# Kernel optimization log

Measured on AMD Instinct MI355X. Metric: run time of the kernel, lower is better.

Reference implementation:

```python
import jax, jax.numpy as jnp
import numpy as np

EPS = 1e-5


def _dwconv(x, w, pad):
    # x: [N,C,H,W]; w: [C,1,k,k] depthwise kernel (groups = C)
    return jax.lax.conv_general_dilated(
        x, w, window_strides=(1, 1), padding=[(pad, pad), (pad, pad)],
        feature_group_count=w.shape[0],
        dimension_numbers=("NCHW", "OIHW", "NCHW"))


def _bn(y, g, b, m, v):
    # inference-mode BatchNorm2d using running stats; per-channel affine
    scale = (g / jnp.sqrt(v + EPS))[None, :, None, None]
    shift = (b - m * g / jnp.sqrt(v + EPS))[None, :, None, None]
    return y * scale + shift


def setup_inputs() -> dict:
    key = jax.random.key(0)
    ks = jax.random.split(key, 16)
    C, KL, KS = 384, 13, 3
    N, H, W = 16, 64, 64
    inp = {
        "x": jax.random.normal(ks[0], (N, C, H, W), jnp.float32),
        "w_large": jax.random.normal(ks[1], (C, 1, KL, KL), jnp.float32) * 0.05,
        "w_small": jax.random.normal(ks[2], (C, 1, KS, KS), jnp.float32) * 0.2,
        "g_l": jax.random.normal(ks[3], (C,), jnp.float32),
        "b_l": jax.random.normal(ks[4], (C,), jnp.float32),
        "m_l": jax.random.normal(ks[5], (C,), jnp.float32),
        "v_l": jax.random.uniform(ks[6], (C,), jnp.float32, 0.5, 1.5),
        "g_s": jax.random.normal(ks[7], (C,), jnp.float32),
        "b_s": jax.random.normal(ks[8], (C,), jnp.float32),
        "m_s": jax.random.normal(ks[9], (C,), jnp.float32),
        "v_s": jax.random.uniform(ks[10], (C,), jnp.float32, 0.5, 1.5),
        "g_i": jax.random.normal(ks[11], (C,), jnp.float32),
        "b_i": jax.random.normal(ks[12], (C,), jnp.float32),
        "m_i": jax.random.normal(ks[13], (C,), jnp.float32),
        "v_i": jax.random.uniform(ks[14], (C,), jnp.float32, 0.5, 1.5),
    }
    return inp


def reference(x, w_large, w_small, g_l, b_l, m_l, v_l,
              g_s, b_s, m_s, v_s, g_i, b_i, m_i, v_i):
    kl = w_large.shape[-1]
    ks = w_small.shape[-1]
    out = (_bn(_dwconv(x, w_large, kl // 2), g_l, b_l, m_l, v_l)
           + _bn(_dwconv(x, w_small, ks // 2), g_s, b_s, m_s, v_s)
           + _bn(x, g_i, b_i, m_i, v_i))
    return out
```

## Files before the change

### kernel.cpp

```cpp
#include <hip/hip_runtime.h>

#define EPSV 1e-5f

typedef __fp16 f16x8 __attribute__((ext_vector_type(8)));
typedef float f32x4 __attribute__((ext_vector_type(4)));
typedef __fp16 half2v __attribute__((ext_vector_type(2)));

__device__ __forceinline__ unsigned h2_as_u32(half2v h) {
    union { half2v h; unsigned u; } cv;
    cv.h = h;
    return cv.u;
}

#define LROWS 76
#define LSTRIDE 88

__global__ __launch_bounds__(256) void fuse_weights(
    const float* __restrict__ w_large, const float* __restrict__ w_small,
    const float* __restrict__ g_l, const float* __restrict__ b_l,
    const float* __restrict__ m_l, const float* __restrict__ v_l,
    const float* __restrict__ g_s, const float* __restrict__ b_s,
    const float* __restrict__ m_s, const float* __restrict__ v_s,
    const float* __restrict__ g_i, const float* __restrict__ b_i,
    const float* __restrict__ m_i, const float* __restrict__ v_i,
    float* __restrict__ bf, uint4* __restrict__ wB) {
    __shared__ float sw[169];
    const int c = blockIdx.x;
    const int t = threadIdx.x;
    const float sl = g_l[c] * rsqrtf(v_l[c] + EPSV);
    const float ss = g_s[c] * rsqrtf(v_s[c] + EPSV);
    const float si = g_i[c] * rsqrtf(v_i[c] + EPSV);
    if (t < 169) {
        const int ky = t / 13, kx = t % 13;
        float w = w_large[c * 169 + t] * sl;
        if (ky >= 5 && ky <= 7 && kx >= 5 && kx <= 7)
            w += w_small[c * 9 + (ky - 5) * 3 + (kx - 5)] * ss;
        if (t == 6 * 13 + 6) w += si;
        sw[t] = w;
    }
    if (t == 0)
        bf[c] = (b_l[c] - m_l[c] * sl) + (b_s[c] - m_s[c] * ss) +
                (b_i[c] - m_i[c] * si);
    __syncthreads();
    for (int it = t; it < 832; it += 256) {
        const int dy = it >> 6;
        const int l = it & 63;
        const int i = l & 15;
        const int kb = (l >> 4) * 8;
        unsigned u[4];
#pragma unroll
        for (int jj = 0; jj < 4; ++jj) {
            const int kx0 = kb + 2 * jj - i - 2;
            const int kx1 = kx0 + 1;
            const float w0 =
                (kx0 >= 0 && kx0 <= 12) ? sw[dy * 13 + kx0] : 0.0f;
            const float w1 =
                (kx1 >= 0 && kx1 <= 12) ? sw[dy * 13 + kx1] : 0.0f;
            u[jj] = h2_as_u32(__builtin_amdgcn_cvt_pkrtz(w0, w1));
        }
        wB[(size_t)c * 832 + it] = make_uint4(u[0], u[1], u[2], u[3]);
    }
}

__global__ __launch_bounds__(256, 6) void dwconv_mfma(
    const float* __restrict__ x, const uint4* __restrict__ wB,
    const float* __restrict__ bf, float* __restrict__ out) {
    __shared__ __align__(16) __fp16 tile[LROWS * LSTRIDE];
    unsigned* tz = (unsigned*)tile;

    const int t = threadIdx.x;
    const int img = blockIdx.x;
    const int c = __builtin_amdgcn_readfirstlane(img % 384);
    const size_t base = (size_t)img * 4096;

    if (t < 120) {
        const int r = t / 10;
        const int rr = (r < 6) ? r : r + 64;
        const int qq = t - r * 10;
        *(uint4*)(tz + rr * 44 + qq * 4) = make_uint4(0u, 0u, 0u, 0u);
    }
    if (t < 128) {
        const int r = 6 + (t >> 1);
        const int sb = (t & 1) ? 36 : 0;
        *(uint4*)(tz + r * 44 + sb) = make_uint4(0u, 0u, 0u, 0u);
    }

    {
        const int r = t >> 2;
        const int q = t & 3;
        const float* src = x + base + r * 64 + q * 16;
        unsigned u[8];
#pragma unroll
        for (int p = 0; p < 4; ++p) {
            const float4 v = ((const float4*)src)[p];
            u[2 * p + 0] = h2_as_u32(__builtin_amdgcn_cvt_pkrtz(v.x, v.y));
            u[2 * p + 1] = h2_as_u32(__builtin_amdgcn_cvt_pkrtz(v.z, v.w));
        }
        unsigned* dst = tz + (r + 6) * 44 + 4 + q * 8;
        *(uint4*)dst = make_uint4(u[0], u[1], u[2], u[3]);
        *(uint4*)(dst + 4) = make_uint4(u[4], u[5], u[6], u[7]);
    }

    const int l = t & 63;
    const int wv = t >> 6;
    const int c0 = wv * 16;
    const int lrow = l & 15;
    const int kb = (l >> 4) * 8;
    const __fp16* abase = tile + lrow * LSTRIDE + c0 + kb;
    const uint4* __restrict__ wbp = wB + (size_t)c * 832 + l;
    const float bv = bf[c];

    uint4 bcur = wbp[0];

    f32x4 acc0 = {bv, bv, bv, bv};
    f32x4 acc1 = {bv, bv, bv, bv};
    f32x4 acc2 = {bv, bv, bv, bv};
    f32x4 acc3 = {bv, bv, bv, bv};

    __syncthreads();

#pragma unroll 1
    for (int dy = 0; dy < 13; ++dy) {
        const int dyn = (dy < 12) ? dy + 1 : 12;
        const uint4 bnext = wbp[dyn * 64];
        union { uint4 u; f16x8 h; } bc;
        bc.u = bcur;
        const f16x8 a0 = *(const f16x8*)(abase + (dy) * LSTRIDE);
        const f16x8 a1 = *(const f16x8*)(abase + (16 + dy) * LSTRIDE);
        const f16x8 a2 = *(const f16x8*)(abase + (32 + dy) * LSTRIDE);
        const f16x8 a3 = *(const f16x8*)(abase + (48 + dy) * LSTRIDE);
        acc0 = __builtin_amdgcn_mfma_f32_16x16x32_f16(a0, bc.h, acc0, 0, 0, 0);
        acc1 = __builtin_amdgcn_mfma_f32_16x16x32_f16(a1, bc.h, acc1, 0, 0, 0);
        acc2 = __builtin_amdgcn_mfma_f32_16x16x32_f16(a2, bc.h, acc2, 0, 0, 0);
        acc3 = __builtin_amdgcn_mfma_f32_16x16x32_f16(a3, bc.h, acc3, 0, 0, 0);
        bcur = bnext;
    }

    const int ocol = c0 + (l & 15);
    const int orow = 4 * (l >> 4);
    float* ob = out + base;
#pragma unroll
    for (int q = 0; q < 4; ++q) {
        ob[(orow + q) * 64 + ocol] = acc0[q];
        ob[(16 + orow + q) * 64 + ocol] = acc1[q];
        ob[(32 + orow + q) * 64 + ocol] = acc2[q];
        ob[(48 + orow + q) * 64 + ocol] = acc3[q];
    }
}

extern "C" void kernel_launch(void* const* d_in, const int* in_sizes, int n_in,
                              void* d_out, int out_size, void* d_ws,
                              size_t ws_size, hipStream_t stream) {
    const float* x = (const float*)d_in[0];
    const float* w_large = (const float*)d_in[1];
    const float* w_small = (const float*)d_in[2];
    const float* g_l = (const float*)d_in[3];
    const float* b_l = (const float*)d_in[4];
    const float* m_l = (const float*)d_in[5];
    const float* v_l = (const float*)d_in[6];
    const float* g_s = (const float*)d_in[7];
    const float* b_s = (const float*)d_in[8];
    const float* m_s = (const float*)d_in[9];
    const float* v_s = (const float*)d_in[10];
    const float* g_i = (const float*)d_in[11];
    const float* b_i = (const float*)d_in[12];
    const float* m_i = (const float*)d_in[13];
    const float* v_i = (const float*)d_in[14];
    float* outp = (float*)d_out;

    float* bfp = (float*)d_ws;
    uint4* wB = (uint4*)(bfp + 384);

    fuse_weights<<<384, 256, 0, stream>>>(w_large, w_small, g_l, b_l, m_l, v_l,
                                          g_s, b_s, m_s, v_s, g_i, b_i, m_i,
                                          v_i, bfp, wB);
    dwconv_mfma<<<16 * 384, 256, 0, stream>>>(x, wB, bfp, outp);
}
```

Measured before the change: 47.21 us.

## Process four images per block with double-buffered LDS and register-resident weights

Each block now handles four images of the same channel instead of one. The 13 weight fragments are loaded once into registers and reused across the images. Input tiles are double-buffered in LDS so the global load and fp16 conversion of the next image overlap the MFMA work on the current one. This trades higher register and LDS use (occupancy hint lowered to 3) for less per-block setup and better latency hiding in a largely bandwidth-bound kernel.

```diff
diff --git a/kernel.cpp b/kernel.cpp
--- a/kernel.cpp
+++ b/kernel.cpp
@@ -13,7 +13,8 @@
 }
 
 #define LROWS 76
-#define LSTRIDE 88
+#define LSTR32 44
+#define LBUF (LROWS * LSTR32)
 
 __global__ __launch_bounds__(256) void fuse_weights(
     const float* __restrict__ w_large, const float* __restrict__ w_small,
@@ -62,90 +63,128 @@
     }
 }
 
-__global__ __launch_bounds__(256, 6) void dwconv_mfma(
+__global__ __launch_bounds__(256, 3) void dwconv_mfma(
     const float* __restrict__ x, const uint4* __restrict__ wB,
     const float* __restrict__ bf, float* __restrict__ out) {
-    __shared__ __align__(16) __fp16 tile[LROWS * LSTRIDE];
-    unsigned* tz = (unsigned*)tile;
+    __shared__ __align__(16) unsigned lds[2 * LBUF];
 
     const int t = threadIdx.x;
-    const int img = blockIdx.x;
-    const int c = __builtin_amdgcn_readfirstlane(img % 384);
-    const size_t base = (size_t)img * 4096;
-
-    if (t < 120) {
-        const int r = t / 10;
-        const int rr = (r < 6) ? r : r + 64;
-        const int qq = t - r * 10;
-        *(uint4*)(tz + rr * 44 + qq * 4) = make_uint4(0u, 0u, 0u, 0u);
-    }
-    if (t < 128) {
-        const int r = 6 + (t >> 1);
-        const int sb = (t & 1) ? 36 : 0;
-        *(uint4*)(tz + r * 44 + sb) = make_uint4(0u, 0u, 0u, 0u);
-    }
-
-    {
-        const int r = t >> 2;
-        const int q = t & 3;
-        const float* src = x + base + r * 64 + q * 16;
-        unsigned u[8];
-#pragma unroll
-        for (int p = 0; p < 4; ++p) {
-            const float4 v = ((const float4*)src)[p];
-            u[2 * p + 0] = h2_as_u32(__builtin_amdgcn_cvt_pkrtz(v.x, v.y));
-            u[2 * p + 1] = h2_as_u32(__builtin_amdgcn_cvt_pkrtz(v.z, v.w));
-        }
-        unsigned* dst = tz + (r + 6) * 44 + 4 + q * 8;
-        *(uint4*)dst = make_uint4(u[0], u[1], u[2], u[3]);
-        *(uint4*)(dst + 4) = make_uint4(u[4], u[5], u[6], u[7]);
+    const int bid = blockIdx.x;
+    const int c = bid >> 2;
+    const int n0 = (bid & 3) << 2;
+    const size_t base0 = ((size_t)n0 * 384 + c) * 4096;
+    const size_t istep = (size_t)384 * 4096;
+
+#pragma unroll
+    for (int b = 0; b < 2; ++b) {
+        unsigned* tz = lds + b * LBUF;
+        if (t < 120) {
+            const int r = t / 10;
+            const int rr = (r < 6) ? r : r + 64;
+            const int qq = t - r * 10;
+            *(uint4*)(tz + rr * LSTR32 + qq * 4) = make_uint4(0u, 0u, 0u, 0u);
+        }
+        if (t < 128) {
+            const int r = 6 + (t >> 1);
+            const int sb = (t & 1) ? 36 : 0;
+            *(uint4*)(tz + r * LSTR32 + sb) = make_uint4(0u, 0u, 0u, 0u);
+        }
     }
 
     const int l = t & 63;
     const int wv = t >> 6;
+    const float bv = bf[c];
+
+    f16x8 Bf[13];
+    {
+        const uint4* wbp = wB + (size_t)c * 832 + l;
+#pragma unroll
+        for (int dy = 0; dy < 13; ++dy) {
+            union { uint4 u; f16x8 h; } cv;
+            cv.u = wbp[dy * 64];
+            Bf[dy] = cv.h;
+        }
+    }
+
+    const int sr = t >> 2;
+    const int sq = t & 3;
+    const float* srcb = x + base0 + sr * 64 + sq * 16;
+    unsigned* dstA = lds + (sr + 6) * LSTR32 + 4 + sq * 8;
+    unsigned* dstB = lds + LBUF + (sr + 6) * LSTR32 + 4 + sq * 8;
+
+    float4 xr0, xr1, xr2, xr3;
+
+#define ISSUE(k_)                                                      \
+    {                                                                  \
+        const float4* s_ = (const float4*)(srcb + (size_t)(k_)*istep); \
+        xr0 = s_[0]; xr1 = s_[1]; xr2 = s_[2]; xr3 = s_[3];            \
+    }
+
+#define WRITEBUF(d_)                                                   \
+    {                                                                  \
+        unsigned u_[8];                                                \
+        u_[0] = h2_as_u32(__builtin_amdgcn_cvt_pkrtz(xr0.x, xr0.y));   \
+        u_[1] = h2_as_u32(__builtin_amdgcn_cvt_pkrtz(xr0.z, xr0.w));   \
+        u_[2] = h2_as_u32(__builtin_amdgcn_cvt_pkrtz(xr1.x, xr1.y));   \
+        u_[3] = h2_as_u32(__builtin_amdgcn_cvt_pkrtz(xr1.z, xr1.w));   \
+        u_[4] = h2_as_u32(__builtin_amdgcn_cvt_pkrtz(xr2.x, xr2.y));   \
+        u_[5] = h2_as_u32(__builtin_amdgcn_cvt_pkrtz(xr2.z, xr2.w));   \
+        u_[6] = h2_as_u32(__builtin_amdgcn_cvt_pkrtz(xr3.x, xr3.y));   \
+        u_[7] = h2_as_u32(__builtin_amdgcn_cvt_pkrtz(xr3.z, xr3.w));   \
+        *(uint4*)(d_) = make_uint4(u_[0], u_[1], u_[2], u_[3]);        \
+        *(uint4*)((d_) + 4) = make_uint4(u_[4], u_[5], u_[6], u_[7]);  \
+    }
+
+    ISSUE(0);
+    WRITEBUF(dstA);
+    ISSUE(1);
+    __syncthreads();
+
     const int c0 = wv * 16;
     const int lrow = l & 15;
     const int kb = (l >> 4) * 8;
-    const __fp16* abase = tile + lrow * LSTRIDE + c0 + kb;
-    const uint4* __restrict__ wbp = wB + (size_t)c * 832 + l;
-    const float bv = bf[c];
-
-    uint4 bcur = wbp[0];
-
-    f32x4 acc0 = {bv, bv, bv, bv};
-    f32x4 acc1 = {bv, bv, bv, bv};
-    f32x4 acc2 = {bv, bv, bv, bv};
-    f32x4 acc3 = {bv, bv, bv, bv};
-
-    __syncthreads();
-
-#pragma unroll 1
-    for (int dy = 0; dy < 13; ++dy) {
-        const int dyn = (dy < 12) ? dy + 1 : 12;
-        const uint4 bnext = wbp[dyn * 64];
-        union { uint4 u; f16x8 h; } bc;
-        bc.u = bcur;
-        const f16x8 a0 = *(const f16x8*)(abase + (dy) * LSTRIDE);
-        const f16x8 a1 = *(const f16x8*)(abase + (16 + dy) * LSTRIDE);
-        const f16x8 a2 = *(const f16x8*)(abase + (32 + dy) * LSTRIDE);
-        const f16x8 a3 = *(const f16x8*)(abase + (48 + dy) * LSTRIDE);
-        acc0 = __builtin_amdgcn_mfma_f32_16x16x32_f16(a0, bc.h, acc0, 0, 0, 0);
-        acc1 = __builtin_amdgcn_mfma_f32_16x16x32_f16(a1, bc.h, acc1, 0, 0, 0);
-        acc2 = __builtin_amdgcn_mfma_f32_16x16x32_f16(a2, bc.h, acc2, 0, 0, 0);
-        acc3 = __builtin_amdgcn_mfma_f32_16x16x32_f16(a3, bc.h, acc3, 0, 0, 0);
-        bcur = bnext;
-    }
-
     const int ocol = c0 + (l & 15);
     const int orow = 4 * (l >> 4);
-    float* ob = out + base;
-#pragma unroll
-    for (int q = 0; q < 4; ++q) {
-        ob[(orow + q) * 64 + ocol] = acc0[q];
-        ob[(16 + orow + q) * 64 + ocol] = acc1[q];
-        ob[(32 + orow + q) * 64 + ocol] = acc2[q];
-        ob[(48 + orow + q) * 64 + ocol] = acc3[q];
-    }
+    const __fp16* ab0 = (const __fp16*)lds + lrow * 88 + c0 + kb;
+    const __fp16* ab1 = (const __fp16*)(lds + LBUF) + lrow * 88 + c0 + kb;
+
+#pragma unroll
+    for (int k = 0; k < 4; ++k) {
+        const int cur = k & 1;
+        if (k < 3) {
+            if (cur == 0) { WRITEBUF(dstB); } else { WRITEBUF(dstA); }
+        }
+        if (k < 2) ISSUE(k + 2);
+
+        const __fp16* ab = cur ? ab1 : ab0;
+        f32x4 acc0 = {bv, bv, bv, bv};
+        f32x4 acc1 = {bv, bv, bv, bv};
+        f32x4 acc2 = {bv, bv, bv, bv};
+        f32x4 acc3 = {bv, bv, bv, bv};
+#pragma unroll
+        for (int dy = 0; dy < 13; ++dy) {
+            const f16x8 a0 = *(const f16x8*)(ab + (dy) * 88);
+            const f16x8 a1 = *(const f16x8*)(ab + (16 + dy) * 88);
+            const f16x8 a2 = *(const f16x8*)(ab + (32 + dy) * 88);
+            const f16x8 a3 = *(const f16x8*)(ab + (48 + dy) * 88);
+            acc0 = __builtin_amdgcn_mfma_f32_16x16x32_f16(a0, Bf[dy], acc0, 0, 0, 0);
+            acc1 = __builtin_amdgcn_mfma_f32_16x16x32_f16(a1, Bf[dy], acc1, 0, 0, 0);
+            acc2 = __builtin_amdgcn_mfma_f32_16x16x32_f16(a2, Bf[dy], acc2, 0, 0, 0);
+            acc3 = __builtin_amdgcn_mfma_f32_16x16x32_f16(a3, Bf[dy], acc3, 0, 0, 0);
+        }
+
+        float* ob = out + base0 + (size_t)k * istep;
+#pragma unroll
+        for (int q = 0; q < 4; ++q) {
+            ob[(orow + q) * 64 + ocol] = acc0[q];
+            ob[(16 + orow + q) * 64 + ocol] = acc1[q];
+            ob[(32 + orow + q) * 64 + ocol] = acc2[q];
+            ob[(48 + orow + q) * 64 + ocol] = acc3[q];
+        }
+        if (k < 3) __syncthreads();
+    }
+#undef ISSUE
+#undef WRITEBUF
 }
 
 extern "C" void kernel_launch(void* const* d_in, const int* in_sizes, int n_in,
@@ -174,5 +213,5 @@
     fuse_weights<<<384, 256, 0, stream>>>(w_large, w_small, g_l, b_l, m_l, v_l,
                                           g_s, b_s, m_s, v_s, g_i, b_i, m_i,
                                           v_i, bfp, wB);
-    dwconv_mfma<<<16 * 384, 256, 0, stream>>>(x, wB, bfp, outp);
-}
+    dwconv_mfma<<<1536, 256, 0, stream>>>(x, wB, bfp, outp);
+}
```

Result: faster. 44.32 us (-6.1%).
